# Kernel tuning notes

Hardware: AMD Instinct MI355X
Metric: run time of the kernel (lower is better)

The kernel has to match this reference:

```python
import jax, jax.numpy as jnp
import numpy as np

B, T, D = 16, 512, 512
MEL_MAX = 4096


def setup_inputs() -> dict:
    key = jax.random.key(0)
    k0, k1, k2, k3 = jax.random.split(key, 4)
    x = jax.random.normal(k0, (B, T, D), dtype=jnp.float32)
    # integer frame durations per phoneme (the `target` used in training-mode LR)
    target = jax.random.randint(k1, (B, T), 0, 8, dtype=jnp.int32)
    scale = 1.0 / np.sqrt(D)
    W1 = jax.random.normal(k2, (D, D), dtype=jnp.float32) * scale
    b1 = jnp.zeros((D,), dtype=jnp.float32)
    W2 = jax.random.normal(k3, (D, 1), dtype=jnp.float32) * scale
    b2 = jnp.zeros((1,), dtype=jnp.float32)
    return {"x": x, "W1": W1, "b1": b1, "W2": W2, "b2": b2,
            "target": target, "mel_max_length": MEL_MAX}


def _length_regulate(x, durations, mel_max_length):
    """Vectorized repeat_interleave + pad.
    x: [B,T,D] float, durations: [B,T] int, output: [B,mel_max_length,D].
    Equivalent to per-batch torch expand+cat then pad, done via cumsum+searchsorted gather.
    """
    cs = jnp.cumsum(durations, axis=1)                    # [B,T] exclusive upper bounds
    pos = jnp.arange(mel_max_length)                      # [L]

    def expand_one(xb, csb):
        idx = jnp.searchsorted(csb, pos, side='right')    # [L] phoneme index per frame
        valid = pos < csb[-1]                             # frames beyond total -> pad
        idx = jnp.clip(idx, 0, xb.shape[0] - 1)
        return jnp.where(valid[:, None], xb[idx], jnp.zeros((), xb.dtype))

    return jax.vmap(expand_one)(x, cs)                    # [B,L,D]


def reference(x, W1, b1, W2, b2, target, mel_max_length):
    # DurationPredictor: Linear(512,512)+ReLU, Linear(512,1)+ReLU, squeeze -> [B,T]
    h = jax.nn.relu(jnp.einsum('btd,de->bte', x, W1) + b1)
    duration_predictor_output = jax.nn.relu(jnp.einsum('bte,eo->bto', h, W2) + b2)[..., 0]
    # Training-mode LR: expand x by integer `target` durations, pad to mel_max_length
    output = _length_regulate(x, target, mel_max_length)
    return output, duration_predictor_output
```

## Files before the change

### kernel.cpp

```cpp
#include <hip/hip_runtime.h>
#include <hip/hip_bf16.h>

#define BSZ 16
#define TT 512
#define DD 512
#define MM (BSZ * TT)
#define NCB 4
#define NPART (NCB * 2)
#define NGEMM 256

typedef __attribute__((ext_vector_type(8))) short bf16x8;
typedef __attribute__((ext_vector_type(4))) float f32x4;

__global__ __launch_bounds__(256) void prep_kernel(const float* __restrict__ x,
                                                   const float* __restrict__ W1,
                                                   const int* __restrict__ target,
                                                   ushort* __restrict__ xh,
                                                   ushort* __restrict__ wth,
                                                   int* __restrict__ imap, int L) {
    int bid = blockIdx.x;
    if (bid < 4096) {
        int i = bid * 256 + threadIdx.x;
        float4 v = ((const float4*)x)[i];
        float f[4] = {v.x, v.y, v.z, v.w};
        ushort hh[4];
        #pragma unroll
        for (int j = 0; j < 4; ++j) {
            __hip_bfloat16 bh = __float2bfloat16(f[j]);
            hh[j] = *(ushort*)&bh;
        }
        ((ushort4*)xh)[i] = make_ushort4(hh[0], hh[1], hh[2], hh[3]);
    } else if (bid < 4352) {
        int t = (bid - 4096) * 256 + threadIdx.x;
        int n  = t & (DD - 1);
        int kq = t >> 9;
        ushort hh[4];
        #pragma unroll
        for (int i = 0; i < 4; ++i) {
            float f = W1[(size_t)(kq * 4 + i) * DD + n];
            __hip_bfloat16 bh = __float2bfloat16(f);
            hh[i] = *(ushort*)&bh;
        }
        ((ushort4*)wth)[(size_t)n * (DD / 4) + kq] = make_ushort4(hh[0], hh[1], hh[2], hh[3]);
    } else {
        int b = bid - 4352;
        __shared__ int s[TT];
        int t = threadIdx.x;
        s[t]       = target[b * TT + t];
        s[t + 256] = target[b * TT + t + 256];
        __syncthreads();
        #pragma unroll
        for (int off = 1; off < TT; off <<= 1) {
            int v0 = (t >= off) ? s[t - off] : 0;
            int v1 = s[t + 256 - off];
            __syncthreads();
            s[t] += v0;
            s[t + 256] += v1;
            __syncthreads();
        }
        int total = s[TT - 1];
        int* imb = imap + (size_t)b * L;
        for (int ph = t; ph < TT; ph += 256) {
            int st = (ph == 0) ? 0 : s[ph - 1];
            int en = s[ph];
            for (int d = st; d < en; ++d) imb[d] = ph;
        }
        for (int l = total + t; l < L; l += 256) imb[l] = -1;
    }
}

#define BM 128
#define BN 128
#define BK 64
__global__ __launch_bounds__(256) void mega_kernel(const ushort* __restrict__ xh,
                                                   const ushort* __restrict__ wth,
                                                   const float* __restrict__ b1,
                                                   const float* __restrict__ W2,
                                                   const float* __restrict__ x,
                                                   const int* __restrict__ imap,
                                                   float* __restrict__ out,
                                                   float* __restrict__ partial,
                                                   int L) {
    __shared__ ushort lds[2][2][128 * 64];
    const int bid = blockIdx.x;
    const int t = threadIdx.x;
    const int lane = t & 63, wave = t >> 6;
    const int row0 = (bid >> 2) * BM;
    const int col0 = (bid & 3) * BN;
    const int rq = t >> 3;
    const int ls = (t & 7) ^ (rq & 7);
    const int sco = ls * 8;

    const int b_lr    = bid >> 4;
    const int chunk0  = (bid & 15) * 256;
    const int lr_lane = t & 127;
    const int lr_half = t >> 7;
    const float4* x4g = (const float4*)(x + (size_t)b_lr * TT * DD);
    float4*       o4  = (float4*)(out + (size_t)b_lr * L * DD);
    const int*    imb = imap + (size_t)b_lr * L;

    auto stage = [&](int buf, int kt) {
        const int k0 = kt * BK;
        #pragma unroll
        for (int q = 0; q < 4; ++q) {
            int row = q * 32 + rq;
            const ushort* ga = xh + (size_t)(row0 + row) * DD + k0 + sco;
            auto la = (__attribute__((address_space(3))) unsigned int*)
                      ((char*)&lds[buf][0][0] + q * 4096 + wave * 1024);
            __builtin_amdgcn_global_load_lds(
                (const __attribute__((address_space(1))) unsigned int*)ga, la, 16, 0, 0);
        }
        #pragma unroll
        for (int q = 0; q < 4; ++q) {
            int row = q * 32 + rq;
            const ushort* gb = wth + (size_t)(col0 + row) * DD + k0 + sco;
            auto lb = (__attribute__((address_space(3))) unsigned int*)
                      ((char*)&lds[buf][1][0] + q * 4096 + wave * 1024);
            __builtin_amdgcn_global_load_lds(
                (const __attribute__((address_space(1))) unsigned int*)gb, lb, 16, 0, 0);
        }
    };

    const int wm = (wave >> 1) * 64;
    const int wn = (wave & 1) * 64;
    const int l15 = lane & 15, l4 = lane >> 4;
    f32x4 acc[4][4] = {};

    stage(0, 0);
    __syncthreads();
    int cur = 0;
    #pragma unroll 1
    for (int kt = 0; kt < DD / BK; ++kt) {
        if (kt + 1 < DD / BK) stage(cur ^ 1, kt + 1);

        const int rb0 = chunk0 + kt * 32 + lr_half;
        int idx0[8];
        #pragma unroll
        for (int p = 0; p < 8; ++p) idx0[p] = imb[rb0 + p * 2];
        float4 gv[8];
        #pragma unroll
        for (int p = 0; p < 8; ++p)
            gv[p] = (idx0[p] >= 0) ? x4g[(size_t)idx0[p] * (DD / 4) + lr_lane]
                                   : make_float4(0.f, 0.f, 0.f, 0.f);

        const ushort* At = &lds[cur][0][0];
        const ushort* Bt = &lds[cur][1][0];
        bf16x8 a[4][2], b[4][2];
        #pragma unroll
        for (int i = 0; i < 4; ++i) {
            int r = wm + i * 16 + l15;
            #pragma unroll
            for (int ks = 0; ks < 2; ++ks) {
                int sl = (ks * 4 + l4) ^ (r & 7);
                a[i][ks] = *(const bf16x8*)&At[r * 64 + sl * 8];
            }
        }
        #pragma unroll
        for (int j = 0; j < 4; ++j) {
            int r = wn + j * 16 + l15;
            #pragma unroll
            for (int ks = 0; ks < 2; ++ks) {
                int sl = (ks * 4 + l4) ^ (r & 7);
                b[j][ks] = *(const bf16x8*)&Bt[r * 64 + sl * 8];
            }
        }

        #pragma unroll
        for (int i = 0; i < 4; ++i)
            #pragma unroll
            for (int j = 0; j < 4; ++j)
                acc[i][j] = __builtin_amdgcn_mfma_f32_16x16x32_bf16(a[i][0], b[j][0], acc[i][j], 0, 0, 0);

        #pragma unroll
        for (int p = 0; p < 8; ++p)
            o4[(size_t)(rb0 + p * 2) * (DD / 4) + lr_lane] = gv[p];
        const int rb1 = rb0 + 16;
        int idx1[8];
        #pragma unroll
        for (int p = 0; p < 8; ++p) idx1[p] = imb[rb1 + p * 2];
        #pragma unroll
        for (int p = 0; p < 8; ++p)
            gv[p] = (idx1[p] >= 0) ? x4g[(size_t)idx1[p] * (DD / 4) + lr_lane]
                                   : make_float4(0.f, 0.f, 0.f, 0.f);

        #pragma unroll
        for (int i = 0; i < 4; ++i)
            #pragma unroll
            for (int j = 0; j < 4; ++j)
                acc[i][j] = __builtin_amdgcn_mfma_f32_16x16x32_bf16(a[i][1], b[j][1], acc[i][j], 0, 0, 0);

        #pragma unroll
        for (int p = 0; p < 8; ++p)
            o4[(size_t)(rb1 + p * 2) * (DD / 4) + lr_lane] = gv[p];

        __syncthreads();
        cur ^= 1;
    }

    const int pslice = (bid & 3) * 2 + (wn >> 6);
    #pragma unroll
    for (int i = 0; i < 4; ++i) {
        #pragma unroll
        for (int r = 0; r < 4; ++r) {
            float s = 0.f;
            #pragma unroll
            for (int j = 0; j < 4; ++j) {
                int cg = col0 + wn + j * 16 + l15;
                float h = acc[i][j][r] + b1[cg];
                h = fmaxf(h, 0.f);
                s += h * W2[cg];
            }
            s += __shfl_xor(s, 1);
            s += __shfl_xor(s, 2);
            s += __shfl_xor(s, 4);
            s += __shfl_xor(s, 8);
            if (l15 == 0) {
                int rg = row0 + wm + i * 16 + l4 * 4 + r;
                partial[(size_t)pslice * MM + rg] = s;
            }
        }
    }
}

__global__ __launch_bounds__(256) void dpo_kernel(const float* __restrict__ partial,
                                                  const float* __restrict__ b2,
                                                  float* __restrict__ dpo) {
    int m = blockIdx.x * 256 + threadIdx.x;
    float s = b2[0];
    #pragma unroll
    for (int nb = 0; nb < NPART; ++nb) s += partial[(size_t)nb * MM + m];
    dpo[m] = fmaxf(s, 0.f);
}

extern "C" void kernel_launch(void* const* d_in, const int* in_sizes, int n_in,
                              void* d_out, int out_size, void* d_ws, size_t ws_size,
                              hipStream_t stream) {
    const float* x      = (const float*)d_in[0];
    const float* W1     = (const float*)d_in[1];
    const float* b1     = (const float*)d_in[2];
    const float* W2     = (const float*)d_in[3];
    const float* b2     = (const float*)d_in[4];
    const int*   target = (const int*)d_in[5];
    int L = (out_size - BSZ * TT) / (BSZ * DD);

    float* out_lr  = (float*)d_out;
    float* out_dpo = (float*)d_out + (size_t)BSZ * L * DD;

    ushort* xh      = (ushort*)d_ws;
    ushort* wth     = xh + (size_t)MM * DD;
    float*  partial = (float*)(wth + (size_t)DD * DD);
    int*    imap    = (int*)(partial + (size_t)NPART * MM);

    prep_kernel<<<dim3(4368), dim3(256), 0, stream>>>(x, W1, target, xh, wth, imap, L);
    mega_kernel<<<dim3(NGEMM), dim3(256), 0, stream>>>(xh, wth, b1, W2,
                                                       x, imap, out_lr, partial, L);
    dpo_kernel<<<dim3(MM / 256), dim3(256), 0, stream>>>(partial, b2, out_dpo);
}
```

Before: 44.44 us.

## Fuse x bf16 conversion into GEMM A-staging and halve GEMM tile rows

Drops the separate pass that converted x to bf16 in the prep kernel. The mega kernel now loads fp32 x rows directly, converts them in registers and writes swizzled bf16 into LDS. BM is halved to 64 so the grid doubles to 512 blocks with launch_bounds(256,2), and the length-regulation copy is split across more blocks using nontemporal stores. This removes a full read/write pass over x and the intermediate buffer. In exchange, A-staging becomes synchronous register loads instead of async global-to-LDS loads, and W1 tiles are reloaded more often.

```diff
diff --git a/kernel.cpp b/kernel.cpp
--- a/kernel.cpp
+++ b/kernel.cpp
@@ -5,33 +5,20 @@
 #define TT 512
 #define DD 512
 #define MM (BSZ * TT)
-#define NCB 4
-#define NPART (NCB * 2)
-#define NGEMM 256
+#define NPART 8
+#define NMEGA 512
 
 typedef __attribute__((ext_vector_type(8))) short bf16x8;
+typedef __attribute__((ext_vector_type(8))) unsigned short ushort8;
 typedef __attribute__((ext_vector_type(4))) float f32x4;
 
-__global__ __launch_bounds__(256) void prep_kernel(const float* __restrict__ x,
-                                                   const float* __restrict__ W1,
+__global__ __launch_bounds__(256) void prep_kernel(const float* __restrict__ W1,
                                                    const int* __restrict__ target,
-                                                   ushort* __restrict__ xh,
                                                    ushort* __restrict__ wth,
                                                    int* __restrict__ imap, int L) {
     int bid = blockIdx.x;
-    if (bid < 4096) {
-        int i = bid * 256 + threadIdx.x;
-        float4 v = ((const float4*)x)[i];
-        float f[4] = {v.x, v.y, v.z, v.w};
-        ushort hh[4];
-        #pragma unroll
-        for (int j = 0; j < 4; ++j) {
-            __hip_bfloat16 bh = __float2bfloat16(f[j]);
-            hh[j] = *(ushort*)&bh;
-        }
-        ((ushort4*)xh)[i] = make_ushort4(hh[0], hh[1], hh[2], hh[3]);
-    } else if (bid < 4352) {
-        int t = (bid - 4096) * 256 + threadIdx.x;
+    if (bid < 256) {
+        int t = bid * 256 + threadIdx.x;
         int n  = t & (DD - 1);
         int kq = t >> 9;
         ushort hh[4];
@@ -43,7 +30,7 @@
         }
         ((ushort4*)wth)[(size_t)n * (DD / 4) + kq] = make_ushort4(hh[0], hh[1], hh[2], hh[3]);
     } else {
-        int b = bid - 4352;
+        int b = bid - 256;
         __shared__ int s[TT];
         int t = threadIdx.x;
         s[t]       = target[b * TT + t];
@@ -69,19 +56,19 @@
     }
 }
 
-#define BM 128
+#define BM 64
 #define BN 128
 #define BK 64
-__global__ __launch_bounds__(256) void mega_kernel(const ushort* __restrict__ xh,
-                                                   const ushort* __restrict__ wth,
-                                                   const float* __restrict__ b1,
-                                                   const float* __restrict__ W2,
-                                                   const float* __restrict__ x,
-                                                   const int* __restrict__ imap,
-                                                   float* __restrict__ out,
-                                                   float* __restrict__ partial,
-                                                   int L) {
-    __shared__ ushort lds[2][2][128 * 64];
+__global__ __launch_bounds__(256, 2) void mega_kernel(const ushort* __restrict__ wth,
+                                                      const float* __restrict__ b1,
+                                                      const float* __restrict__ W2,
+                                                      const float* __restrict__ x,
+                                                      const int* __restrict__ imap,
+                                                      float* __restrict__ out,
+                                                      float* __restrict__ partial,
+                                                      int L) {
+    __shared__ ushort ldsA[2][BM * 64];
+    __shared__ ushort ldsB[2][BN * 64];
     const int bid = blockIdx.x;
     const int t = threadIdx.x;
     const int lane = t & 63, wave = t >> 6;
@@ -90,64 +77,76 @@
     const int rq = t >> 3;
     const int ls = (t & 7) ^ (rq & 7);
     const int sco = ls * 8;
-
-    const int b_lr    = bid >> 4;
-    const int chunk0  = (bid & 15) * 256;
+    const int ar = t >> 2;
+    const int ac = (t & 3) * 16;
+
+    const int b_lr    = bid >> 5;
+    const int chunk0  = (bid & 31) * 128;
     const int lr_lane = t & 127;
     const int lr_half = t >> 7;
-    const float4* x4g = (const float4*)(x + (size_t)b_lr * TT * DD);
-    float4*       o4  = (float4*)(out + (size_t)b_lr * L * DD);
-    const int*    imb = imap + (size_t)b_lr * L;
-
-    auto stage = [&](int buf, int kt) {
+    const f32x4* x4g = (const f32x4*)(x + (size_t)b_lr * TT * DD);
+    f32x4*       o4  = (f32x4*)(out + (size_t)b_lr * L * DD);
+    const int*   imb = imap + (size_t)b_lr * L;
+
+    auto stageB = [&](int buf, int kt) {
         const int k0 = kt * BK;
-        #pragma unroll
-        for (int q = 0; q < 4; ++q) {
-            int row = q * 32 + rq;
-            const ushort* ga = xh + (size_t)(row0 + row) * DD + k0 + sco;
-            auto la = (__attribute__((address_space(3))) unsigned int*)
-                      ((char*)&lds[buf][0][0] + q * 4096 + wave * 1024);
-            __builtin_amdgcn_global_load_lds(
-                (const __attribute__((address_space(1))) unsigned int*)ga, la, 16, 0, 0);
-        }
         #pragma unroll
         for (int q = 0; q < 4; ++q) {
             int row = q * 32 + rq;
             const ushort* gb = wth + (size_t)(col0 + row) * DD + k0 + sco;
             auto lb = (__attribute__((address_space(3))) unsigned int*)
-                      ((char*)&lds[buf][1][0] + q * 4096 + wave * 1024);
+                      ((char*)&ldsB[buf][0] + q * 4096 + wave * 1024);
             __builtin_amdgcn_global_load_lds(
                 (const __attribute__((address_space(1))) unsigned int*)gb, lb, 16, 0, 0);
         }
     };
-
-    const int wm = (wave >> 1) * 64;
+    auto stageA = [&](int buf, int kt) {
+        const float* xa = x + (size_t)(row0 + ar) * DD + kt * BK + ac;
+        float fl[16];
+        *(f32x4*)&fl[0]  = ((const f32x4*)xa)[0];
+        *(f32x4*)&fl[4]  = ((const f32x4*)xa)[1];
+        *(f32x4*)&fl[8]  = ((const f32x4*)xa)[2];
+        *(f32x4*)&fl[12] = ((const f32x4*)xa)[3];
+        ushort us[16];
+        #pragma unroll
+        for (int j = 0; j < 16; ++j) {
+            __hip_bfloat16 bh = __float2bfloat16(fl[j]);
+            us[j] = *(ushort*)&bh;
+        }
+        int s0 = ((t & 3) * 2)     ^ (ar & 7);
+        int s1 = ((t & 3) * 2 + 1) ^ (ar & 7);
+        *(ushort8*)&ldsA[buf][ar * 64 + s0 * 8] = *(ushort8*)&us[0];
+        *(ushort8*)&ldsA[buf][ar * 64 + s1 * 8] = *(ushort8*)&us[8];
+    };
+
+    const int wm = (wave >> 1) * 32;
     const int wn = (wave & 1) * 64;
     const int l15 = lane & 15, l4 = lane >> 4;
-    f32x4 acc[4][4] = {};
-
-    stage(0, 0);
+    f32x4 acc[2][4] = {};
+
+    stageB(0, 0);
+    stageA(0, 0);
     __syncthreads();
     int cur = 0;
     #pragma unroll 1
     for (int kt = 0; kt < DD / BK; ++kt) {
-        if (kt + 1 < DD / BK) stage(cur ^ 1, kt + 1);
-
-        const int rb0 = chunk0 + kt * 32 + lr_half;
-        int idx0[8];
-        #pragma unroll
-        for (int p = 0; p < 8; ++p) idx0[p] = imb[rb0 + p * 2];
-        float4 gv[8];
+        if (kt + 1 < DD / BK) stageB(cur ^ 1, kt + 1);
+
+        const int rb0 = chunk0 + kt * 16 + lr_half;
+        int idxs[8];
+        #pragma unroll
+        for (int p = 0; p < 8; ++p) idxs[p] = imb[rb0 + p * 2];
+        f32x4 gv[8];
         #pragma unroll
         for (int p = 0; p < 8; ++p)
-            gv[p] = (idx0[p] >= 0) ? x4g[(size_t)idx0[p] * (DD / 4) + lr_lane]
-                                   : make_float4(0.f, 0.f, 0.f, 0.f);
-
-        const ushort* At = &lds[cur][0][0];
-        const ushort* Bt = &lds[cur][1][0];
-        bf16x8 a[4][2], b[4][2];
-        #pragma unroll
-        for (int i = 0; i < 4; ++i) {
+            gv[p] = (idxs[p] >= 0) ? x4g[(size_t)idxs[p] * (DD / 4) + lr_lane]
+                                   : (f32x4){0.f, 0.f, 0.f, 0.f};
+
+        const ushort* At = &ldsA[cur][0];
+        const ushort* Bt = &ldsB[cur][0];
+        bf16x8 a[2][2], b[4][2];
+        #pragma unroll
+        for (int i = 0; i < 2; ++i) {
             int r = wm + i * 16 + l15;
             #pragma unroll
             for (int ks = 0; ks < 2; ++ks) {
@@ -164,34 +163,19 @@
                 b[j][ks] = *(const bf16x8*)&Bt[r * 64 + sl * 8];
             }
         }
-
-        #pragma unroll
-        for (int i = 0; i < 4; ++i)
-            #pragma unroll
-            for (int j = 0; j < 4; ++j)
-                acc[i][j] = __builtin_amdgcn_mfma_f32_16x16x32_bf16(a[i][0], b[j][0], acc[i][j], 0, 0, 0);
+        #pragma unroll
+        for (int ks = 0; ks < 2; ++ks)
+            #pragma unroll
+            for (int i = 0; i < 2; ++i)
+                #pragma unroll
+                for (int j = 0; j < 4; ++j)
+                    acc[i][j] = __builtin_amdgcn_mfma_f32_16x16x32_bf16(a[i][ks], b[j][ks], acc[i][j], 0, 0, 0);
+
+        if (kt + 1 < DD / BK) stageA(cur ^ 1, kt + 1);
 
         #pragma unroll
         for (int p = 0; p < 8; ++p)
-            o4[(size_t)(rb0 + p * 2) * (DD / 4) + lr_lane] = gv[p];
-        const int rb1 = rb0 + 16;
-        int idx1[8];
-        #pragma unroll
-        for (int p = 0; p < 8; ++p) idx1[p] = imb[rb1 + p * 2];
-        #pragma unroll
-        for (int p = 0; p < 8; ++p)
-            gv[p] = (idx1[p] >= 0) ? x4g[(size_t)idx1[p] * (DD / 4) + lr_lane]
-                                   : make_float4(0.f, 0.f, 0.f, 0.f);
-
-        #pragma unroll
-        for (int i = 0; i < 4; ++i)
-            #pragma unroll
-            for (int j = 0; j < 4; ++j)
-                acc[i][j] = __builtin_amdgcn_mfma_f32_16x16x32_bf16(a[i][1], b[j][1], acc[i][j], 0, 0, 0);
-
-        #pragma unroll
-        for (int p = 0; p < 8; ++p)
-            o4[(size_t)(rb1 + p * 2) * (DD / 4) + lr_lane] = gv[p];
+            __builtin_nontemporal_store(gv[p], &o4[(size_t)(rb0 + p * 2) * (DD / 4) + lr_lane]);
 
         __syncthreads();
         cur ^= 1;
@@ -199,7 +183,7 @@
 
     const int pslice = (bid & 3) * 2 + (wn >> 6);
     #pragma unroll
-    for (int i = 0; i < 4; ++i) {
+    for (int i = 0; i < 2; ++i) {
         #pragma unroll
         for (int r = 0; r < 4; ++r) {
             float s = 0.f;
@@ -246,13 +230,12 @@
     float* out_lr  = (float*)d_out;
     float* out_dpo = (float*)d_out + (size_t)BSZ * L * DD;
 
-    ushort* xh      = (ushort*)d_ws;
-    ushort* wth     = xh + (size_t)MM * DD;
+    ushort* wth     = (ushort*)d_ws;
     float*  partial = (float*)(wth + (size_t)DD * DD);
     int*    imap    = (int*)(partial + (size_t)NPART * MM);
 
-    prep_kernel<<<dim3(4368), dim3(256), 0, stream>>>(x, W1, target, xh, wth, imap, L);
-    mega_kernel<<<dim3(NGEMM), dim3(256), 0, stream>>>(xh, wth, b1, W2,
-                                                       x, imap, out_lr, partial, L);
+    prep_kernel<<<dim3(272), dim3(256), 0, stream>>>(W1, target, wth, imap, L);
+    mega_kernel<<<dim3(NMEGA), dim3(256), 0, stream>>>(wth, b1, W2, x, imap,
+                                                       out_lr, partial, L);
     dpo_kernel<<<dim3(MM / 256), dim3(256), 0, stream>>>(partial, b2, out_dpo);
 }
```

Result: faster. 43.04 us (-3.2%).
